# Optimization experiments

Hardware: AMD Instinct MI355X
Metric: run time of the kernel (lower is better)

The kernel has to match this reference:

```python
import jax, jax.numpy as jnp
import numpy as np

DIM = 768
CA = 192  # int(dim * mlp_ratio)
T = 8

def setup_inputs() -> dict:
    key = jax.random.key(0)
    ks = jax.random.split(key, 7)
    x = jax.random.normal(ks[0], (197, 128, DIM), dtype=jnp.float32)
    w1 = jax.random.normal(ks[1], (DIM, CA), dtype=jnp.float32) * 0.02
    b1 = jax.random.normal(ks[2], (CA,), dtype=jnp.float32) * 0.02
    conv_w = jax.random.normal(ks[3], (CA, 3), dtype=jnp.float32) * 0.02  # depthwise temporal kernel (3,1,1)
    conv_b = jax.random.normal(ks[4], (CA,), dtype=jnp.float32) * 0.02
    w2 = jax.random.normal(ks[5], (CA, DIM), dtype=jnp.float32) * 0.02
    b2 = jax.random.normal(ks[6], (DIM,), dtype=jnp.float32) * 0.02
    return {"x": x, "w1": w1, "b1": b1, "conv_w": conv_w, "conv_b": conv_b, "w2": w2, "b2": b2}

def reference(x, w1, b1, conv_w, conv_b, w2, b2):
    # x: (L, BT, dim), tokens-first layout (fc1 applied before permute)
    x_id = x
    h = x @ w1 + b1                      # (L, BT, Ca)
    h = jnp.transpose(h, (1, 0, 2))      # (BT, L, Ca)
    BT, L, Ca = h.shape
    B = BT // T
    h = h[:, 1:, :]                      # drop first token (L-1 patch tokens)
    x_cls = h[:, :1, :]                  # (BT, 1, Ca) -- first token AFTER the slice (as in original)
    x_temp = h.reshape(B, T, L - 1, Ca)  # (B, T, P, Ca)
    # Depthwise Conv3d with kernel (3,1,1), pad (1,0,0): pure temporal depthwise conv.
    xp = jnp.pad(x_temp, ((0, 0), (1, 1), (0, 0), (0, 0)))
    x_after = (xp[:, :-2] * conv_w[:, 0] + xp[:, 1:-1] * conv_w[:, 1]
               + xp[:, 2:] * conv_w[:, 2] + conv_b)  # (B, T, P, Ca)
    # Triangular-masked pairwise diff: sum_{i<j} (x_after[j] - x_temp[i]) / 28,
    # computed without materializing the (B,T,T,P,Ca) diff tensor:
    # each x_after[j] appears j times; each x_temp[i] appears (T-1-i) times.
    t = jnp.arange(T, dtype=x.dtype)
    result = (jnp.einsum('t,btpc->bpc', t, x_after)
              - jnp.einsum('t,btpc->bpc', (T - 1) - t, x_temp)) / 28.0
    x_last = (x_temp + result[:, None]).reshape(BT, L - 1, Ca)
    out = jnp.concatenate([x_cls, x_last], axis=1)   # (BT, L, Ca)
    out = jnp.transpose(out, (1, 0, 2))              # (L, BT, Ca)
    out = jax.nn.gelu(out, approximate=False)        # torch nn.GELU default = exact erf
    out = out @ w2 + b2                              # (L, BT, dim)
    return x_id + out
```

## Files before the change

kernel.cpp:

```cpp
#include <hip/hip_runtime.h>
#include <hip/hip_bf16.h>
#include <math.h>

#define L_TOK 197
#define BTOK  128
#define DIM   768
#define CA    192
#define M_ROWS (L_TOK * BTOK)

typedef __attribute__((ext_vector_type(8))) short  short8;
typedef __attribute__((ext_vector_type(4))) short  short4v;
typedef __attribute__((ext_vector_type(4))) float  f32x4;
typedef __attribute__((ext_vector_type(4))) float  float4v;

static __device__ __forceinline__ short f2bf(float f) {
    union { __hip_bfloat16 b; short s; } u;
    u.b = __float2bfloat16(f);
    return u.s;
}

static __device__ __forceinline__ float gelu_exact(float x) {
    return 0.5f * x * (1.0f + erff(x * 0.70710678118654752440f));
}

__global__ void prep_kernel(const float* __restrict__ w1, const float* __restrict__ w2,
                            short* __restrict__ w1T, short* __restrict__ w2T) {
    int idx = blockIdx.x * 256 + threadIdx.x;
    if (idx < CA * DIM) {
        int n = idx / DIM, k = idx - n * DIM;
        w1T[idx] = f2bf(w1[k * CA + n]);
        int n2 = idx / CA, k2 = idx - n2 * CA;
        w2T[idx] = f2bf(w2[k2 * DIM + n2]);
    }
}

__global__ __launch_bounds__(256) void gemm1_kernel(
        const float* __restrict__ x, const short* __restrict__ w1T,
        const float* __restrict__ b1, float* __restrict__ h) {
    __shared__ __align__(16) short As[32][40];
    __shared__ __align__(16) short Bs[192][40];

    const int tid  = threadIdx.x;
    const int m0   = blockIdx.x * 32;
    const int wave = tid >> 6, lane = tid & 63;
    const int wm = wave >> 1, wn = wave & 1;
    const int lm = lane & 15;
    const int lk = (lane >> 4) * 8;

    const int arow  = tid >> 3;
    const int akoff = (tid & 7) * 4;
    const int brow  = tid >> 2;
    const int bkoff = (tid & 3) * 8;

    f32x4 acc[6] = {};

    for (int k0 = 0; k0 < DIM; k0 += 32) {
        float4v av = *(const float4v*)(x + (m0 + arow) * DIM + k0 + akoff);
        short4v a4;
        #pragma unroll
        for (int i = 0; i < 4; i++) a4[i] = f2bf(av[i]);
        short8 bv[3];
        #pragma unroll
        for (int i = 0; i < 3; i++)
            bv[i] = *(const short8*)(w1T + (i * 64 + brow) * DIM + k0 + bkoff);

        __syncthreads();
        *(short4v*)&As[arow][akoff] = a4;
        #pragma unroll
        for (int i = 0; i < 3; i++)
            *(short8*)&Bs[i * 64 + brow][bkoff] = bv[i];
        __syncthreads();

        short8 af = *(const short8*)&As[wm * 16 + lm][lk];
        #pragma unroll
        for (int j = 0; j < 6; j++) {
            short8 bf = *(const short8*)&Bs[wn * 96 + j * 16 + lm][lk];
            acc[j] = __builtin_amdgcn_mfma_f32_16x16x32_bf16(af, bf, acc[j], 0, 0, 0);
        }
    }

    const int row0 = m0 + wm * 16 + (lane >> 4) * 4;
    #pragma unroll
    for (int j = 0; j < 6; j++) {
        int col = wn * 96 + j * 16 + lm;
        float bias = b1[col];
        #pragma unroll
        for (int r = 0; r < 4; r++)
            h[(row0 + r) * CA + col] = acc[j][r] + bias;
    }
}

__global__ void mid_kernel(const float* __restrict__ h, const float* __restrict__ conv_w,
                           const float* __restrict__ conv_b, short* __restrict__ g) {
    const int c = threadIdx.x;
    const int b = blockIdx.x;
    const int p = blockIdx.y;
    const int l = p + 1;

    const float cw0 = conv_w[c * 3 + 0];
    const float cw1 = conv_w[c * 3 + 1];
    const float cw2 = conv_w[c * 3 + 2];
    const float cb  = conv_b[c];

    const float* hp = h + (l * BTOK + b * 8) * CA + c;
    float hv[8];
    #pragma unroll
    for (int t = 0; t < 8; t++) hv[t] = hp[t * CA];

    float s = 0.f;
    #pragma unroll
    for (int t = 0; t < 8; t++) {
        float coef = (float)t * cw1 - (float)(7 - t);
        if (t <= 6) coef += (float)(t + 1) * cw0;
        if (t >= 1) coef += (float)(t - 1) * cw2;
        s += coef * hv[t];
    }
    const float res = cb + s * (1.0f / 28.0f);

    short* gp = g + (l * BTOK + b * 8) * CA + c;
    #pragma unroll
    for (int t = 0; t < 8; t++) gp[t * CA] = f2bf(gelu_exact(hv[t] + res));

    if (p == 0) {
        short* g0 = g + (b * 8) * CA + c;
        #pragma unroll
        for (int t = 0; t < 8; t++) g0[t * CA] = f2bf(gelu_exact(hv[t]));
    }
}

__global__ __launch_bounds__(256) void gemm2_kernel(
        const short* __restrict__ g, const short* __restrict__ w2T,
        const float* __restrict__ b2, const float* __restrict__ x,
        float* __restrict__ out) {
    __shared__ __align__(16) short As[64][40];
    __shared__ __align__(16) short Bs[128][40];

    const int tid  = threadIdx.x;
    const int m0   = blockIdx.x * 64;
    const int n0   = blockIdx.y * 128;
    const int wave = tid >> 6, lane = tid & 63;
    const int wm = wave >> 1, wn = wave & 1;
    const int lm = lane & 15;
    const int lk = (lane >> 4) * 8;

    const int arow = tid >> 2;
    const int koff = (tid & 3) * 8;

    f32x4 acc[2][4] = {};

    for (int k0 = 0; k0 < CA; k0 += 32) {
        short8 av  = *(const short8*)(g   + (m0 + arow) * CA + k0 + koff);
        short8 bv0 = *(const short8*)(w2T + (n0 + arow) * CA + k0 + koff);
        short8 bv1 = *(const short8*)(w2T + (n0 + 64 + arow) * CA + k0 + koff);

        __syncthreads();
        *(short8*)&As[arow][koff]      = av;
        *(short8*)&Bs[arow][koff]      = bv0;
        *(short8*)&Bs[64 + arow][koff] = bv1;
        __syncthreads();

        short8 af0 = *(const short8*)&As[wm * 32 + lm][lk];
        short8 af1 = *(const short8*)&As[wm * 32 + 16 + lm][lk];
        #pragma unroll
        for (int j = 0; j < 4; j++) {
            short8 bf = *(const short8*)&Bs[wn * 64 + j * 16 + lm][lk];
            acc[0][j] = __builtin_amdgcn_mfma_f32_16x16x32_bf16(af0, bf, acc[0][j], 0, 0, 0);
            acc[1][j] = __builtin_amdgcn_mfma_f32_16x16x32_bf16(af1, bf, acc[1][j], 0, 0, 0);
        }
    }

    #pragma unroll
    for (int i = 0; i < 2; i++) {
        const int row0 = m0 + wm * 32 + i * 16 + (lane >> 4) * 4;
        #pragma unroll
        for (int j = 0; j < 4; j++) {
            int col = n0 + wn * 64 + j * 16 + lm;
            float bias = b2[col];
            #pragma unroll
            for (int r = 0; r < 4; r++) {
                int idx = (row0 + r) * DIM + col;
                out[idx] = acc[i][j][r] + x[idx] + bias;
            }
        }
    }
}

extern "C" void kernel_launch(void* const* d_in, const int* in_sizes, int n_in,
                              void* d_out, int out_size, void* d_ws, size_t ws_size,
                              hipStream_t stream) {
    (void)in_sizes; (void)n_in; (void)out_size; (void)ws_size;
    const float* x      = (const float*)d_in[0];
    const float* w1     = (const float*)d_in[1];
    const float* b1     = (const float*)d_in[2];
    const float* conv_w = (const float*)d_in[3];
    const float* conv_b = (const float*)d_in[4];
    const float* w2     = (const float*)d_in[5];
    const float* b2     = (const float*)d_in[6];
    float* out = (float*)d_out;

    char* ws = (char*)d_ws;
    float* h   = (float*)ws;
    short* g   = (short*)(ws + 19365888);
    short* w1T = (short*)(ws + 19365888 + 9682944);
    short* w2T = (short*)(ws + 19365888 + 9682944 + 294912);

    prep_kernel<<<(CA * DIM + 255) / 256, 256, 0, stream>>>(w1, w2, w1T, w2T);
    gemm1_kernel<<<M_ROWS / 32, 256, 0, stream>>>(x, w1T, b1, h);
    mid_kernel<<<dim3(16, 196), CA, 0, stream>>>(h, conv_w, conv_b, g);
    gemm2_kernel<<<dim3(M_ROWS / 64, DIM / 128), 256, 0, stream>>>(g, w2T, b2, x, out);
}
```

Baseline: 220.1 us.

## Fuse temporal conv and GELU into GEMM1 epilogue; async LDS loads

Merges the mid kernel into the first GEMM's epilogue. Each block now owns one token position's 64 rows, which are 8 full temporal groups, so the conv/diff reduction is done with a cross-lane shuffle. This removes the fp32 intermediate h write and read and one launch. Both GEMMs now use direct global-to-LDS loads into double-buffered, XOR-swizzled tiles, and GEMM2 uses a larger K tile. GEMM1 work for row l=0 is skipped because it is never needed, but the block count of 784 and larger per-block tiles may reduce occupancy.

```diff
diff --git a/kernel.cpp b/kernel.cpp
--- a/kernel.cpp
+++ b/kernel.cpp
@@ -2,25 +2,24 @@
 #include <hip/hip_bf16.h>
 #include <math.h>
 
-#define L_TOK 197
-#define BTOK  128
 #define DIM   768
 #define CA    192
-#define M_ROWS (L_TOK * BTOK)
-
-typedef __attribute__((ext_vector_type(8))) short  short8;
-typedef __attribute__((ext_vector_type(4))) short  short4v;
-typedef __attribute__((ext_vector_type(4))) float  f32x4;
-typedef __attribute__((ext_vector_type(4))) float  float4v;
+#define NTOK  25216
+
+typedef __attribute__((ext_vector_type(8))) short short8;
+typedef __attribute__((ext_vector_type(4))) float f32x4;
 
 static __device__ __forceinline__ short f2bf(float f) {
     union { __hip_bfloat16 b; short s; } u;
     u.b = __float2bfloat16(f);
     return u.s;
 }
-
 static __device__ __forceinline__ float gelu_exact(float x) {
     return 0.5f * x * (1.0f + erff(x * 0.70710678118654752440f));
+}
+static __device__ __forceinline__ void ld16(void* lds, const void* gsrc) {
+    __builtin_amdgcn_global_load_lds((const __attribute__((address_space(1))) void*)gsrc,
+                                     (__attribute__((address_space(3))) void*)lds, 16, 0, 0);
 }
 
 __global__ void prep_kernel(const float* __restrict__ w1, const float* __restrict__ w2,
@@ -34,152 +33,203 @@
     }
 }
 
-__global__ __launch_bounds__(256) void gemm1_kernel(
+__global__ __launch_bounds__(256) void gemm1_fused(
         const float* __restrict__ x, const short* __restrict__ w1T,
-        const float* __restrict__ b1, float* __restrict__ h) {
-    __shared__ __align__(16) short As[32][40];
-    __shared__ __align__(16) short Bs[192][40];
-
-    const int tid  = threadIdx.x;
-    const int m0   = blockIdx.x * 32;
+        const float* __restrict__ b1, const float* __restrict__ conv_w,
+        const float* __restrict__ conv_b, short* __restrict__ gq) {
+    __shared__ __align__(16) short As[64 * 40];
+    __shared__ __align__(16) short Bs[2][96 * 32];
+
+    const int tid = threadIdx.x;
+    const int bx  = blockIdx.x;
+    const int l   = (bx >> 2) + 1;
+    const int hm  = (bx >> 1) & 1;
+    const int n0  = (bx & 1) * 96;
+    const int R0  = l * 128 + hm * 64;
+
     const int wave = tid >> 6, lane = tid & 63;
     const int wm = wave >> 1, wn = wave & 1;
-    const int lm = lane & 15;
-    const int lk = (lane >> 4) * 8;
-
-    const int arow  = tid >> 3;
-    const int akoff = (tid & 7) * 4;
-    const int brow  = tid >> 2;
-    const int bkoff = (tid & 3) * 8;
-
-    f32x4 acc[6] = {};
-
-    for (int k0 = 0; k0 < DIM; k0 += 32) {
-        float4v av = *(const float4v*)(x + (m0 + arow) * DIM + k0 + akoff);
-        short4v a4;
-        #pragma unroll
-        for (int i = 0; i < 4; i++) a4[i] = f2bf(av[i]);
-        short8 bv[3];
-        #pragma unroll
-        for (int i = 0; i < 3; i++)
-            bv[i] = *(const short8*)(w1T + (i * 64 + brow) * DIM + k0 + bkoff);
-
+    const int lm = lane & 15, lg = lane >> 4;
+    const int lk = lg * 8;
+
+    const int arow = tid >> 2;
+    const int acol = (tid & 3) * 8;
+    const float* xrow = x + (size_t)(R0 + arow) * DIM + acol;
+
+    f32x4 acc[2][3] = {};
+
+    f32x4 av0 = *(const f32x4*)(xrow);
+    f32x4 av1 = *(const f32x4*)(xrow + 4);
+    if (wave < 3) {
+        #pragma unroll
+        for (int j = 0; j < 2; j++) {
+            int s = (wave * 2 + j) * 64 + lane;
+            int m = s >> 2;
+            int q = (s & 3) ^ ((m >> 1) & 3);
+            ld16(&Bs[0][(wave * 2 + j) * 512], w1T + (size_t)(n0 + m) * DIM + q * 8);
+        }
+    }
+
+    for (int i = 0; i < 24; i++) {
+        const int p = i & 1;
+        short8 a8;
+        #pragma unroll
+        for (int e = 0; e < 4; e++) { a8[e] = f2bf(av0[e]); a8[4 + e] = f2bf(av1[e]); }
         __syncthreads();
-        *(short4v*)&As[arow][akoff] = a4;
-        #pragma unroll
-        for (int i = 0; i < 3; i++)
-            *(short8*)&Bs[i * 64 + brow][bkoff] = bv[i];
+        *(short8*)&As[arow * 40 + acol] = a8;
         __syncthreads();
-
-        short8 af = *(const short8*)&As[wm * 16 + lm][lk];
-        #pragma unroll
-        for (int j = 0; j < 6; j++) {
-            short8 bf = *(const short8*)&Bs[wn * 96 + j * 16 + lm][lk];
-            acc[j] = __builtin_amdgcn_mfma_f32_16x16x32_bf16(af, bf, acc[j], 0, 0, 0);
-        }
-    }
-
-    const int row0 = m0 + wm * 16 + (lane >> 4) * 4;
-    #pragma unroll
-    for (int j = 0; j < 6; j++) {
-        int col = wn * 96 + j * 16 + lm;
-        float bias = b1[col];
-        #pragma unroll
-        for (int r = 0; r < 4; r++)
-            h[(row0 + r) * CA + col] = acc[j][r] + bias;
-    }
-}
-
-__global__ void mid_kernel(const float* __restrict__ h, const float* __restrict__ conv_w,
-                           const float* __restrict__ conv_b, short* __restrict__ g) {
-    const int c = threadIdx.x;
-    const int b = blockIdx.x;
-    const int p = blockIdx.y;
-    const int l = p + 1;
-
-    const float cw0 = conv_w[c * 3 + 0];
-    const float cw1 = conv_w[c * 3 + 1];
-    const float cw2 = conv_w[c * 3 + 2];
-    const float cb  = conv_b[c];
-
-    const float* hp = h + (l * BTOK + b * 8) * CA + c;
-    float hv[8];
-    #pragma unroll
-    for (int t = 0; t < 8; t++) hv[t] = hp[t * CA];
-
-    float s = 0.f;
-    #pragma unroll
-    for (int t = 0; t < 8; t++) {
-        float coef = (float)t * cw1 - (float)(7 - t);
-        if (t <= 6) coef += (float)(t + 1) * cw0;
-        if (t >= 1) coef += (float)(t - 1) * cw2;
-        s += coef * hv[t];
-    }
-    const float res = cb + s * (1.0f / 28.0f);
-
-    short* gp = g + (l * BTOK + b * 8) * CA + c;
-    #pragma unroll
-    for (int t = 0; t < 8; t++) gp[t * CA] = f2bf(gelu_exact(hv[t] + res));
-
-    if (p == 0) {
-        short* g0 = g + (b * 8) * CA + c;
-        #pragma unroll
-        for (int t = 0; t < 8; t++) g0[t * CA] = f2bf(gelu_exact(hv[t]));
+        if (i < 23) {
+            const float* xn = xrow + (i + 1) * 32;
+            av0 = *(const f32x4*)(xn);
+            av1 = *(const f32x4*)(xn + 4);
+            if (wave < 3) {
+                const int k0n = (i + 1) * 32;
+                #pragma unroll
+                for (int j = 0; j < 2; j++) {
+                    int s = (wave * 2 + j) * 64 + lane;
+                    int m = s >> 2;
+                    int q = (s & 3) ^ ((m >> 1) & 3);
+                    ld16(&Bs[1 - p][(wave * 2 + j) * 512],
+                         w1T + (size_t)(n0 + m) * DIM + k0n + q * 8);
+                }
+            }
+        }
+        short8 af[2], bf[3];
+        af[0] = *(const short8*)&As[(wm * 32 + lm) * 40 + lk];
+        af[1] = *(const short8*)&As[(wm * 32 + 16 + lm) * 40 + lk];
+        #pragma unroll
+        for (int j = 0; j < 3; j++) {
+            int rB = wn * 48 + j * 16 + lm;
+            int qs = lg ^ ((rB >> 1) & 3);
+            bf[j] = *(const short8*)&Bs[p][rB * 32 + qs * 8];
+        }
+        #pragma unroll
+        for (int i2 = 0; i2 < 2; i2++)
+            #pragma unroll
+            for (int j = 0; j < 3; j++)
+                acc[i2][j] = __builtin_amdgcn_mfma_f32_16x16x32_bf16(af[i2], bf[j], acc[i2][j], 0, 0, 0);
+    }
+
+    const int g1 = lg & 1;
+    #pragma unroll
+    for (int j = 0; j < 3; j++) {
+        const int c = n0 + wn * 48 + j * 16 + lm;
+        const float b1c = b1[c];
+        const float cw0 = conv_w[c * 3 + 0];
+        const float cw1 = conv_w[c * 3 + 1];
+        const float cw2 = conv_w[c * 3 + 2];
+        const float cb  = conv_b[c];
+        #pragma unroll
+        for (int i2 = 0; i2 < 2; i2++) {
+            float hv[4];
+            #pragma unroll
+            for (int r = 0; r < 4; r++) hv[r] = acc[i2][j][r] + b1c;
+            float partial = 0.f;
+            #pragma unroll
+            for (int r = 0; r < 4; r++) {
+                const int t = g1 * 4 + r;
+                const float tf = (float)t;
+                float coef = tf * cw1 - (7.0f - tf);
+                if (t <= 6) coef += (tf + 1.0f) * cw0;
+                if (t >= 1) coef += (tf - 1.0f) * cw2;
+                partial += coef * hv[r];
+            }
+            const float full = partial + __shfl_xor(partial, 16);
+            const float res = cb + full * (1.0f / 28.0f);
+            const int row = R0 + wm * 32 + i2 * 16 + lg * 4;
+            #pragma unroll
+            for (int r = 0; r < 4; r++)
+                gq[(size_t)(row + r) * CA + c] = f2bf(gelu_exact(hv[r] + res));
+            if (l == 1) {
+                const int bt = row - 128;
+                #pragma unroll
+                for (int r = 0; r < 4; r++)
+                    gq[(size_t)(bt + r) * CA + c] = f2bf(gelu_exact(hv[r]));
+            }
+        }
     }
 }
 
 __global__ __launch_bounds__(256) void gemm2_kernel(
-        const short* __restrict__ g, const short* __restrict__ w2T,
+        const short* __restrict__ gq, const short* __restrict__ w2T,
         const float* __restrict__ b2, const float* __restrict__ x,
         float* __restrict__ out) {
-    __shared__ __align__(16) short As[64][40];
-    __shared__ __align__(16) short Bs[128][40];
-
-    const int tid  = threadIdx.x;
-    const int m0   = blockIdx.x * 64;
-    const int n0   = blockIdx.y * 128;
+    __shared__ __align__(16) short As[2][64 * 64];
+    __shared__ __align__(16) short Bs[2][128 * 64];
+
+    const int tid = threadIdx.x;
+    const int m0 = blockIdx.x * 64;
+    const int n0 = blockIdx.y * 128;
     const int wave = tid >> 6, lane = tid & 63;
     const int wm = wave >> 1, wn = wave & 1;
-    const int lm = lane & 15;
-    const int lk = (lane >> 4) * 8;
-
-    const int arow = tid >> 2;
-    const int koff = (tid & 3) * 8;
+    const int lm = lane & 15, lg = lane >> 4;
 
     f32x4 acc[2][4] = {};
 
-    for (int k0 = 0; k0 < CA; k0 += 32) {
-        short8 av  = *(const short8*)(g   + (m0 + arow) * CA + k0 + koff);
-        short8 bv0 = *(const short8*)(w2T + (n0 + arow) * CA + k0 + koff);
-        short8 bv1 = *(const short8*)(w2T + (n0 + 64 + arow) * CA + k0 + koff);
-
+    #pragma unroll
+    for (int j = 0; j < 2; j++) {
+        int s = (wave * 2 + j) * 64 + lane;
+        int m = s >> 3, q = (s & 7) ^ (m & 7);
+        ld16(&As[0][(wave * 2 + j) * 512], gq + (size_t)(m0 + m) * CA + q * 8);
+    }
+    #pragma unroll
+    for (int j = 0; j < 4; j++) {
+        int s = (wave * 4 + j) * 64 + lane;
+        int m = s >> 3, q = (s & 7) ^ (m & 7);
+        ld16(&Bs[0][(wave * 4 + j) * 512], w2T + (size_t)(n0 + m) * CA + q * 8);
+    }
+
+    for (int i = 0; i < 3; i++) {
+        const int p = i & 1;
         __syncthreads();
-        *(short8*)&As[arow][koff]      = av;
-        *(short8*)&Bs[arow][koff]      = bv0;
-        *(short8*)&Bs[64 + arow][koff] = bv1;
-        __syncthreads();
-
-        short8 af0 = *(const short8*)&As[wm * 32 + lm][lk];
-        short8 af1 = *(const short8*)&As[wm * 32 + 16 + lm][lk];
+        if (i < 2) {
+            const int k0 = (i + 1) * 64;
+            #pragma unroll
+            for (int j = 0; j < 2; j++) {
+                int s = (wave * 2 + j) * 64 + lane;
+                int m = s >> 3, q = (s & 7) ^ (m & 7);
+                ld16(&As[1 - p][(wave * 2 + j) * 512], gq + (size_t)(m0 + m) * CA + k0 + q * 8);
+            }
+            #pragma unroll
+            for (int j = 0; j < 4; j++) {
+                int s = (wave * 4 + j) * 64 + lane;
+                int m = s >> 3, q = (s & 7) ^ (m & 7);
+                ld16(&Bs[1 - p][(wave * 4 + j) * 512], w2T + (size_t)(n0 + m) * CA + k0 + q * 8);
+            }
+        }
+        #pragma unroll
+        for (int kk = 0; kk < 2; kk++) {
+            const int cb0 = kk * 4 + lg;
+            short8 af[2], bf[4];
+            #pragma unroll
+            for (int i2 = 0; i2 < 2; i2++) {
+                int r = wm * 32 + i2 * 16 + lm;
+                af[i2] = *(const short8*)&As[p][r * 64 + (cb0 ^ (r & 7)) * 8];
+            }
+            #pragma unroll
+            for (int j = 0; j < 4; j++) {
+                int r = wn * 64 + j * 16 + lm;
+                bf[j] = *(const short8*)&Bs[p][r * 64 + (cb0 ^ (r & 7)) * 8];
+            }
+            #pragma unroll
+            for (int i2 = 0; i2 < 2; i2++)
+                #pragma unroll
+                for (int j = 0; j < 4; j++)
+                    acc[i2][j] = __builtin_amdgcn_mfma_f32_16x16x32_bf16(af[i2], bf[j], acc[i2][j], 0, 0, 0);
+        }
+    }
+
+    #pragma unroll
+    for (int i2 = 0; i2 < 2; i2++) {
+        const int row0 = m0 + wm * 32 + i2 * 16 + lg * 4;
         #pragma unroll
         for (int j = 0; j < 4; j++) {
-            short8 bf = *(const short8*)&Bs[wn * 64 + j * 16 + lm][lk];
-            acc[0][j] = __builtin_amdgcn_mfma_f32_16x16x32_bf16(af0, bf, acc[0][j], 0, 0, 0);
-            acc[1][j] = __builtin_amdgcn_mfma_f32_16x16x32_bf16(af1, bf, acc[1][j], 0, 0, 0);
-        }
-    }
-
-    #pragma unroll
-    for (int i = 0; i < 2; i++) {
-        const int row0 = m0 + wm * 32 + i * 16 + (lane >> 4) * 4;
-        #pragma unroll
-        for (int j = 0; j < 4; j++) {
-            int col = n0 + wn * 64 + j * 16 + lm;
-            float bias = b2[col];
+            const int col = n0 + wn * 64 + j * 16 + lm;
+            const float bias = b2[col];
             #pragma unroll
             for (int r = 0; r < 4; r++) {
-                int idx = (row0 + r) * DIM + col;
-                out[idx] = acc[i][j][r] + x[idx] + bias;
+                const size_t idx = (size_t)(row0 + r) * DIM + col;
+                out[idx] = acc[i2][j][r] + x[idx] + bias;
             }
         }
     }
@@ -199,13 +249,11 @@
     float* out = (float*)d_out;
 
     char* ws = (char*)d_ws;
-    float* h   = (float*)ws;
-    short* g   = (short*)(ws + 19365888);
-    short* w1T = (short*)(ws + 19365888 + 9682944);
-    short* w2T = (short*)(ws + 19365888 + 9682944 + 294912);
+    short* g   = (short*)ws;
+    short* w1T = (short*)(ws + 9682944);
+    short* w2T = (short*)(ws + 9682944 + 294912);
 
     prep_kernel<<<(CA * DIM + 255) / 256, 256, 0, stream>>>(w1, w2, w1T, w2T);
-    gemm1_kernel<<<M_ROWS / 32, 256, 0, stream>>>(x, w1T, b1, h);
-    mid_kernel<<<dim3(16, 196), CA, 0, stream>>>(h, conv_w, conv_b, g);
-    gemm2_kernel<<<dim3(M_ROWS / 64, DIM / 128), 256, 0, stream>>>(g, w2T, b2, x, out);
-}
+    gemm1_fused<<<784, 256, 0, stream>>>(x, w1T, b1, conv_w, conv_b, g);
+    gemm2_kernel<<<dim3(394, 6), 256, 0, stream>>>(g, w2T, b2, x, out);
+}
```

After: 195.8 us. 11.0% less time.
